# Performance work log

Measured on AMD Instinct MI355X. Metric: run time of the kernel, lower is better.

The kernel has to match this reference:

```python
import jax, jax.numpy as jnp
import numpy as np
import math

D_MODEL = 1024
N_HEADS = 16
D_HEAD = D_MODEL // N_HEADS  # 64, even (required for RoPE)
MAX_LEN = 1024


def _rope_cache(max_len, d_head, dtype=jnp.float32):
    half = d_head // 2
    inv_freq = jnp.exp(jnp.arange(half, dtype=dtype) * (-math.log(10000.0) / half))
    angles = jnp.arange(max_len, dtype=dtype)[:, None] * inv_freq[None, :]  # [max_len, half]
    return jnp.cos(angles), jnp.sin(angles)


def _apply_rope(t, cos, sin):
    # t: [B, H, L, D]; rotate-by-halves variant (cat of halves, not interleave)
    L = t.shape[2]
    half = t.shape[-1] // 2
    c = cos[:L, :half][None, None, :, :].astype(t.dtype)
    s = sin[:L, :half][None, None, :, :].astype(t.dtype)
    t1, t2 = t[..., :half], t[..., half:]
    return jnp.concatenate([t1 * c - t2 * s, t1 * s + t2 * c], axis=-1)


def setup_inputs() -> dict:
    key = jax.random.key(0)
    ks = jax.random.split(key, 11)
    B, L = 4, 1024
    std = 1.0 / math.sqrt(D_MODEL)
    return {
        "queries": jax.random.normal(ks[0], (B, L, D_MODEL), jnp.float32),
        "keys": jax.random.normal(ks[1], (B, L, D_MODEL), jnp.float32),
        "values": jax.random.normal(ks[2], (B, L, D_MODEL), jnp.float32),
        "Wq": jax.random.normal(ks[3], (D_MODEL, D_MODEL), jnp.float32) * std,
        "bq": jnp.zeros((D_MODEL,), jnp.float32),
        "Wk": jax.random.normal(ks[4], (D_MODEL, D_MODEL), jnp.float32) * std,
        "bk": jnp.zeros((D_MODEL,), jnp.float32),
        "Wv": jax.random.normal(ks[5], (D_MODEL, D_MODEL), jnp.float32) * std,
        "bv": jnp.zeros((D_MODEL,), jnp.float32),
        "Wo": jax.random.normal(ks[6], (D_MODEL, D_MODEL), jnp.float32) * std,
        "bo": jnp.zeros((D_MODEL,), jnp.float32),
    }


def reference(queries, keys, values, Wq, bq, Wk, bk, Wv, bv, Wo, bo):
    B, L, _ = queries.shape
    S = keys.shape[1]
    H, Dh = N_HEADS, D_HEAD
    cos, sin = _rope_cache(MAX_LEN, Dh, queries.dtype)

    q = (queries @ Wq + bq).reshape(B, L, H, Dh).transpose(0, 2, 1, 3)  # [B,H,L,Dh]
    k = (keys @ Wk + bk).reshape(B, S, H, Dh).transpose(0, 2, 1, 3)
    v = (values @ Wv + bv).reshape(B, S, H, Dh).transpose(0, 2, 1, 3)

    q = _apply_rope(q, cos, sin)
    k = _apply_rope(k, cos, sin)

    scores = jnp.einsum('bhid,bhjd->bhij', q, k) / math.sqrt(Dh)
    attn = jax.nn.softmax(scores, axis=-1)  # dropout is identity in eval
    out = jnp.einsum('bhij,bhjd->bhid', attn, v)  # [B,H,L,Dh]
    out = out.transpose(0, 2, 1, 3).reshape(B, L, H * Dh)
    return out @ Wo + bo
```

## Files before the change

kernel.cpp:

```cpp
#include <hip/hip_runtime.h>
#include <math.h>

#define BB 4
#define LL 1024
#define HH 16
#define DH 64
#define DM 1024
#define MM (BB * LL)

typedef short bf16x8 __attribute__((ext_vector_type(8)));
typedef float f32x4  __attribute__((ext_vector_type(4)));
typedef unsigned short u16x4 __attribute__((ext_vector_type(4)));

__device__ __forceinline__ unsigned short f2bf(float x) {
    union { float f; unsigned u; } v; v.f = x;
    unsigned r = v.u + 0x7fff + ((v.u >> 16) & 1);
    return (unsigned short)(r >> 16);
}

__device__ __forceinline__ void gl2lds16(const unsigned short* g, unsigned short* l) {
    __builtin_amdgcn_global_load_lds(
        (const __attribute__((address_space(1))) unsigned int*)g,
        (__attribute__((address_space(3))) unsigned int*)l, 16, 0, 0);
}

__global__ __launch_bounds__(256) void cvt_bf16_kernel(
    const float* __restrict__ i0, const float* __restrict__ i1, const float* __restrict__ i2,
    unsigned short* __restrict__ o0, unsigned short* __restrict__ o1, unsigned short* __restrict__ o2)
{
    int z = blockIdx.z;
    const float* in = (z == 0) ? i0 : (z == 1) ? i1 : i2;
    unsigned short* out = (z == 0) ? o0 : (z == 1) ? o1 : o2;
    int i = (blockIdx.x * 256 + threadIdx.x) * 4;
    float4 f = *(const float4*)(in + i);
    u16x4 r;
    r.x = f2bf(f.x); r.y = f2bf(f.y); r.z = f2bf(f.z); r.w = f2bf(f.w);
    *(u16x4*)(out + i) = r;
}

__global__ __launch_bounds__(256) void transpose_w_kernel(
    const float* __restrict__ w0, const float* __restrict__ w1,
    const float* __restrict__ w2, const float* __restrict__ w3,
    unsigned short* __restrict__ t0, unsigned short* __restrict__ t1,
    unsigned short* __restrict__ t2, unsigned short* __restrict__ t3)
{
    int z = blockIdx.z;
    const float* in = (z == 0) ? w0 : (z == 1) ? w1 : (z == 2) ? w2 : w3;
    unsigned short* out = (z == 0) ? t0 : (z == 1) ? t1 : (z == 2) ? t2 : t3;
    __shared__ float tile[32][33];
    int tx = threadIdx.x & 31, ty = threadIdx.x >> 5;
    int c0 = blockIdx.x * 32, r0 = blockIdx.y * 32;
    #pragma unroll
    for (int j = 0; j < 32; j += 8)
        tile[ty + j][tx] = in[(size_t)(r0 + ty + j) * 1024 + c0 + tx];
    __syncthreads();
    #pragma unroll
    for (int j = 0; j < 32; j += 8)
        out[(size_t)(c0 + ty + j) * 1024 + r0 + tx] = f2bf(tile[tx][ty + j]);
}

__global__ __launch_bounds__(256) void transpose_v_kernel(
    const unsigned short* __restrict__ v, unsigned short* __restrict__ vt)
{
    __shared__ unsigned short T[64][72];
    int bh = blockIdx.y, l0 = blockIdx.x * 64;
    const unsigned short* vg = v + ((size_t)bh * LL + l0) * DH;
    #pragma unroll
    for (int ii = 0; ii < 2; ++ii) {
        int i = ii * 256 + threadIdx.x;
        int r = i >> 3, cb = i & 7;
        bf16x8 vv = *(const bf16x8*)(vg + (size_t)r * DH + cb * 8);
        #pragma unroll
        for (int j = 0; j < 8; ++j)
            T[cb * 8 + j][r] = (unsigned short)vv[j];
    }
    __syncthreads();
    unsigned short* og = vt + (size_t)bh * DH * LL + l0;
    #pragma unroll
    for (int ii = 0; ii < 2; ++ii) {
        int i = ii * 256 + threadIdx.x;
        int d = i >> 3, lb = i & 7;
        *(bf16x8*)(og + (size_t)d * LL + lb * 8) = *(const bf16x8*)&T[d][lb * 8];
    }
}

__device__ __forceinline__ void gemm128_core(
    const unsigned short* __restrict__ A, const unsigned short* __restrict__ Bt,
    unsigned short* As, unsigned short* Bs, int tM, int tN, f32x4 (&acc)[4][4])
{
    const int tid  = threadIdx.x;
    const int wave = tid >> 6, lane = tid & 63;
    const int g = lane >> 4, lm = lane & 15;
    const int wm = wave >> 1, wn = wave & 1;
    const int lr = lane >> 3, lk = lane & 7;
    const int kbl = lk ^ lr;

    for (int kt = 0; kt < 16; ++kt) {
        const int k0 = kt * 64;
        if (kt) __syncthreads();
        #pragma unroll
        for (int it = 0; it < 4; ++it) {
            int rbase = wave * 32 + it * 8;
            int r = rbase + lr;
            gl2lds16(A  + (size_t)(tM + r) * 1024 + k0 + kbl * 8, As + rbase * 64);
            gl2lds16(Bt + (size_t)(tN + r) * 1024 + k0 + kbl * 8, Bs + rbase * 64);
        }
        __syncthreads();

        #pragma unroll
        for (int kk = 0; kk < 2; ++kk) {
            bf16x8 a[4], b[4];
            const int sw = ((kk * 4 + g) ^ (lm & 7)) * 8;
            #pragma unroll
            for (int mt = 0; mt < 4; ++mt)
                a[mt] = *(const bf16x8*)&As[(wm * 64 + mt * 16 + lm) * 64 + sw];
            #pragma unroll
            for (int nt = 0; nt < 4; ++nt)
                b[nt] = *(const bf16x8*)&Bs[(wn * 64 + nt * 16 + lm) * 64 + sw];
            #pragma unroll
            for (int mt = 0; mt < 4; ++mt)
                #pragma unroll
                for (int nt = 0; nt < 4; ++nt)
                    acc[mt][nt] = __builtin_amdgcn_mfma_f32_16x16x32_bf16(
                        a[mt], b[nt], acc[mt][nt], 0, 0, 0);
        }
    }
}

__global__ __launch_bounds__(256) void gemm_qkv_kernel(
    const unsigned short* __restrict__ Aq, const unsigned short* __restrict__ Ak,
    const unsigned short* __restrict__ Av,
    const unsigned short* __restrict__ Wqt, const unsigned short* __restrict__ Wkt,
    const unsigned short* __restrict__ Wvt,
    const float* __restrict__ bq, const float* __restrict__ bk, const float* __restrict__ bv,
    unsigned short* __restrict__ oq, unsigned short* __restrict__ ok,
    unsigned short* __restrict__ ov)
{
    __shared__ __align__(16) unsigned short As[128 * 64];
    __shared__ __align__(16) unsigned short Bs[128 * 64];

    const int z = blockIdx.z;
    const unsigned short* A  = (z == 0) ? Aq  : (z == 1) ? Ak  : Av;
    const unsigned short* Bt = (z == 0) ? Wqt : (z == 1) ? Wkt : Wvt;
    const float* bias        = (z == 0) ? bq  : (z == 1) ? bk  : bv;
    unsigned short* out      = (z == 0) ? oq  : (z == 1) ? ok  : ov;

    const int tM = blockIdx.y * 128, tN = blockIdx.x * 128;
    f32x4 acc[4][4] = {};
    gemm128_core(A, Bt, As, Bs, tM, tN, acc);

    const int wave = threadIdx.x >> 6, lane = threadIdx.x & 63;
    const int g = lane >> 4, lm = lane & 15;
    const int wm = wave >> 1, wn = wave & 1;

    const int colbase = tN + wn * 64;
    const int h = colbase >> 6;
    float bvv[4];
    #pragma unroll
    for (int nt = 0; nt < 4; ++nt) bvv[nt] = bias[colbase + nt * 16 + lm];

    if (z == 2) {
        #pragma unroll
        for (int mt = 0; mt < 4; ++mt)
            #pragma unroll
            for (int r = 0; r < 4; ++r) {
                int row = tM + wm * 64 + mt * 16 + g * 4 + r;
                int b = row >> 10, l = row & 1023;
                unsigned short* orow = out + ((size_t)(b * HH + h) * LL + l) * DH;
                #pragma unroll
                for (int nt = 0; nt < 4; ++nt)
                    orow[nt * 16 + lm] = f2bf(acc[mt][nt][r] + bvv[nt]);
            }
    } else {
        const float coef = -0.28782313662425583f;
        const float if0 = expf((float)lm * coef);
        const float if1 = expf((float)(lm + 16) * coef);
        const float sc  = (z == 0) ? 0.125f * 1.4426950408889634f : 1.0f;
        #pragma unroll
        for (int mt = 0; mt < 4; ++mt)
            #pragma unroll
            for (int r = 0; r < 4; ++r) {
                int row = tM + wm * 64 + mt * 16 + g * 4 + r;
                int b = row >> 10, l = row & 1023;
                unsigned short* orow = out + ((size_t)(b * HH + h) * LL + l) * DH;
                #pragma unroll
                for (int nt = 0; nt < 2; ++nt) {
                    float t1 = acc[mt][nt][r]     + bvv[nt];
                    float t2 = acc[mt][nt + 2][r] + bvv[nt + 2];
                    float ang = (float)l * (nt ? if1 : if0);
                    float s, c;
                    sincosf(ang, &s, &c);
                    orow[nt * 16 + lm]      = f2bf((t1 * c - t2 * s) * sc);
                    orow[nt * 16 + lm + 32] = f2bf((t1 * s + t2 * c) * sc);
                }
            }
    }
}

__global__ __launch_bounds__(256) void gemm_out_kernel(
    const unsigned short* __restrict__ A, const unsigned short* __restrict__ Bt,
    const float* __restrict__ bias, float* __restrict__ C)
{
    __shared__ __align__(16) unsigned short As[128 * 64];
    __shared__ __align__(16) unsigned short Bs[128 * 64];

    const int tM = blockIdx.y * 128, tN = blockIdx.x * 128;
    f32x4 acc[4][4] = {};
    gemm128_core(A, Bt, As, Bs, tM, tN, acc);

    const int wave = threadIdx.x >> 6, lane = threadIdx.x & 63;
    const int g = lane >> 4, lm = lane & 15;
    const int wm = wave >> 1, wn = wave & 1;

    float bvv[4];
    #pragma unroll
    for (int nt = 0; nt < 4; ++nt) bvv[nt] = bias[tN + wn * 64 + nt * 16 + lm];
    #pragma unroll
    for (int mt = 0; mt < 4; ++mt)
        #pragma unroll
        for (int r = 0; r < 4; ++r) {
            int row = tM + wm * 64 + mt * 16 + g * 4 + r;
            float* crow = C + (size_t)row * DM + tN + wn * 64;
            #pragma unroll
            for (int nt = 0; nt < 4; ++nt)
                crow[nt * 16 + lm] = acc[mt][nt][r] + bvv[nt];
        }
}

#define PSTR 72

__global__ __launch_bounds__(256) void attn_mfma_kernel(
    const unsigned short* __restrict__ q, const unsigned short* __restrict__ k,
    const unsigned short* __restrict__ vt, unsigned short* __restrict__ ctx)
{
    __shared__ __align__(16) unsigned short Ks[64 * 64];
    __shared__ __align__(16) unsigned short Vs[64 * 64];
    __shared__ __align__(16) unsigned short Pb[4][16 * PSTR];

    const int tid  = threadIdx.x;
    const int wave = tid >> 6, lane = tid & 63;
    const int g = lane >> 4, lm = lane & 15;
    const int lr = lane >> 3, lk = lane & 7;
    const int kbl = lk ^ lr;
    const int bh = blockIdx.y;
    const int qbase = blockIdx.x * 64;

    const unsigned short* qg  = q  + (size_t)(bh * LL + qbase) * DH;
    const unsigned short* kg  = k  + (size_t)bh * LL * DH;
    const unsigned short* vtg = vt + (size_t)bh * DH * LL;

    bf16x8 aq[2];
    {
        const unsigned short* qrow = qg + (wave * 16 + lm) * DH;
        aq[0] = *(const bf16x8*)(qrow + g * 8);
        aq[1] = *(const bf16x8*)(qrow + 32 + g * 8);
    }

    f32x4 acc[4] = {};
    float lrow[4] = {0.f, 0.f, 0.f, 0.f};

    for (int kt = 0; kt < 16; ++kt) {
        if (kt) __syncthreads();
        #pragma unroll
        for (int it = 0; it < 2; ++it) {
            int rbase = wave * 16 + it * 8;
            int r = rbase + lr;
            gl2lds16(kg  + (size_t)(kt * 64 + r) * DH + kbl * 8, Ks + rbase * 64);
            gl2lds16(vtg + (size_t)r * LL + kt * 64 + kbl * 8,  Vs + rbase * 64);
        }
        __syncthreads();

        f32x4 s[4] = {};
        #pragma unroll
        for (int kk = 0; kk < 2; ++kk) {
            const int sw = ((kk * 4 + g) ^ (lm & 7)) * 8;
            #pragma unroll
            for (int t = 0; t < 4; ++t) {
                bf16x8 bk = *(const bf16x8*)&Ks[(t * 16 + lm) * 64 + sw];
                s[t] = __builtin_amdgcn_mfma_f32_16x16x32_bf16(aq[kk], bk, s[t], 0, 0, 0);
            }
        }

        #pragma unroll
        for (int r = 0; r < 4; ++r) {
            float rs = 0.f;
            #pragma unroll
            for (int t = 0; t < 4; ++t) {
                float p = exp2f(s[t][r]);
                rs += p;
                Pb[wave][(g * 4 + r) * PSTR + t * 16 + lm] = f2bf(p);
            }
            lrow[r] += rs;
        }

        #pragma unroll
        for (int kk = 0; kk < 2; ++kk) {
            bf16x8 ap = *(const bf16x8*)&Pb[wave][lm * PSTR + kk * 32 + g * 8];
            #pragma unroll
            for (int dt = 0; dt < 4; ++dt) {
                bf16x8 bv = *(const bf16x8*)&Vs[(dt * 16 + lm) * 64
                                                + ((kk * 4 + g) ^ (lm & 7)) * 8];
                acc[dt] = __builtin_amdgcn_mfma_f32_16x16x32_bf16(ap, bv, acc[dt], 0, 0, 0);
            }
        }
    }

    int b = bh >> 4, h = bh & 15;
    #pragma unroll
    for (int r = 0; r < 4; ++r) {
        float ts = lrow[r];
        ts += __shfl_xor(ts, 1, 64);
        ts += __shfl_xor(ts, 2, 64);
        ts += __shfl_xor(ts, 4, 64);
        ts += __shfl_xor(ts, 8, 64);
        float inv = 1.f / ts;
        int qrow = qbase + wave * 16 + g * 4 + r;
        unsigned short* orow = ctx + (size_t)(b * LL + qrow) * DM + h * DH;
        #pragma unroll
        for (int dt = 0; dt < 4; ++dt)
            orow[dt * 16 + lm] = f2bf(acc[dt][r] * inv);
    }
}

extern "C" void kernel_launch(void* const* d_in, const int* in_sizes, int n_in,
                              void* d_out, int out_size, void* d_ws, size_t ws_size,
                              hipStream_t stream) {
    const float* queries = (const float*)d_in[0];
    const float* keys    = (const float*)d_in[1];
    const float* values  = (const float*)d_in[2];
    const float* Wq = (const float*)d_in[3];
    const float* bq = (const float*)d_in[4];
    const float* Wk = (const float*)d_in[5];
    const float* bk = (const float*)d_in[6];
    const float* Wv = (const float*)d_in[7];
    const float* bv = (const float*)d_in[8];
    const float* Wo = (const float*)d_in[9];
    const float* bo = (const float*)d_in[10];
    float* out = (float*)d_out;

    unsigned short* qb   = (unsigned short*)d_ws;
    unsigned short* kb_  = qb  + (size_t)MM * DM;
    unsigned short* vb_  = kb_ + (size_t)MM * DM;
    unsigned short* Wqt  = vb_ + (size_t)MM * DM;
    unsigned short* Wkt  = Wqt + (size_t)DM * DM;
    unsigned short* Wvt  = Wkt + (size_t)DM * DM;
    unsigned short* Wot  = Wvt + (size_t)DM * DM;
    unsigned short* q_ws = Wot + (size_t)DM * DM;
    unsigned short* k_ws = q_ws + (size_t)MM * DM;
    unsigned short* v_ws = k_ws + (size_t)MM * DM;
    unsigned short* ctx  = v_ws + (size_t)MM * DM;
    unsigned short* vt   = qb;

    cvt_bf16_kernel<<<dim3(MM * DM / 1024, 1, 3), 256, 0, stream>>>(
        queries, keys, values, qb, kb_, vb_);
    transpose_w_kernel<<<dim3(32, 32, 4), 256, 0, stream>>>(
        Wq, Wk, Wv, Wo, Wqt, Wkt, Wvt, Wot);
    gemm_qkv_kernel<<<dim3(DM / 128, MM / 128, 3), 256, 0, stream>>>(
        qb, kb_, vb_, Wqt, Wkt, Wvt, bq, bk, bv, q_ws, k_ws, v_ws);
    transpose_v_kernel<<<dim3(LL / 64, BB * HH), 256, 0, stream>>>(v_ws, vt);
    attn_mfma_kernel<<<dim3(LL / 64, BB * HH), 256, 0, stream>>>(
        q_ws, k_ws, vt, ctx);
    gemm_out_kernel<<<dim3(DM / 128, MM / 128), 256, 0, stream>>>(
        ctx, Wot, bo, out);
}
```

Measured before the change: 222.9 us.

## Fuse V transpose into QKV epilogue, precompute RoPE table, transpose S tile

The QKV GEMM epilogue now writes V directly in transposed [bh, d, l] layout with vectorized 4-element stores, which removes the separate transpose_v kernel and its round trip through memory. RoPE cos/sin values are precomputed once into a table by an extra z-slice of the convert kernel, replacing per-element sincosf in the epilogue with table loads. The attention kernel swaps the MFMA operands so each lane holds a query column, giving vectorized P stores and a cheaper row-sum reduction. Its grid is flattened so consecutive blocks handle different heads. The RoPE table lives in the ctx buffer, which is safe only because the attention kernel overwrites ctx after the QKV GEMM has finished reading the table.

Measured after the change: 222.3 us. No clear change (-0.3%).

```diff
diff --git a/kernel.cpp b/kernel.cpp
--- a/kernel.cpp
+++ b/kernel.cpp
@@ -26,9 +26,23 @@
 
 __global__ __launch_bounds__(256) void cvt_bf16_kernel(
     const float* __restrict__ i0, const float* __restrict__ i1, const float* __restrict__ i2,
-    unsigned short* __restrict__ o0, unsigned short* __restrict__ o1, unsigned short* __restrict__ o2)
+    unsigned short* __restrict__ o0, unsigned short* __restrict__ o1, unsigned short* __restrict__ o2,
+    float* __restrict__ ct, float* __restrict__ st)
 {
     int z = blockIdx.z;
+    if (z == 3) {
+        int idx = blockIdx.x * 256 + threadIdx.x;
+        if (idx < LL * 32) {
+            int l = idx >> 5, d = idx & 31;
+            const float coef = -0.28782313662425583f;
+            float ang = (float)l * expf((float)d * coef);
+            float s, c;
+            sincosf(ang, &s, &c);
+            ct[idx] = c;
+            st[idx] = s;
+        }
+        return;
+    }
     const float* in = (z == 0) ? i0 : (z == 1) ? i1 : i2;
     unsigned short* out = (z == 0) ? o0 : (z == 1) ? o1 : o2;
     int i = (blockIdx.x * 256 + threadIdx.x) * 4;
@@ -59,31 +73,6 @@
         out[(size_t)(c0 + ty + j) * 1024 + r0 + tx] = f2bf(tile[tx][ty + j]);
 }
 
-__global__ __launch_bounds__(256) void transpose_v_kernel(
-    const unsigned short* __restrict__ v, unsigned short* __restrict__ vt)
-{
-    __shared__ unsigned short T[64][72];
-    int bh = blockIdx.y, l0 = blockIdx.x * 64;
-    const unsigned short* vg = v + ((size_t)bh * LL + l0) * DH;
-    #pragma unroll
-    for (int ii = 0; ii < 2; ++ii) {
-        int i = ii * 256 + threadIdx.x;
-        int r = i >> 3, cb = i & 7;
-        bf16x8 vv = *(const bf16x8*)(vg + (size_t)r * DH + cb * 8);
-        #pragma unroll
-        for (int j = 0; j < 8; ++j)
-            T[cb * 8 + j][r] = (unsigned short)vv[j];
-    }
-    __syncthreads();
-    unsigned short* og = vt + (size_t)bh * DH * LL + l0;
-    #pragma unroll
-    for (int ii = 0; ii < 2; ++ii) {
-        int i = ii * 256 + threadIdx.x;
-        int d = i >> 3, lb = i & 7;
-        *(bf16x8*)(og + (size_t)d * LL + lb * 8) = *(const bf16x8*)&T[d][lb * 8];
-    }
-}
-
 __device__ __forceinline__ void gemm128_core(
     const unsigned short* __restrict__ A, const unsigned short* __restrict__ Bt,
     unsigned short* As, unsigned short* Bs, int tM, int tN, f32x4 (&acc)[4][4])
@@ -133,8 +122,9 @@
     const unsigned short* __restrict__ Wqt, const unsigned short* __restrict__ Wkt,
     const unsigned short* __restrict__ Wvt,
     const float* __restrict__ bq, const float* __restrict__ bk, const float* __restrict__ bv,
+    const float* __restrict__ ct, const float* __restrict__ st,
     unsigned short* __restrict__ oq, unsigned short* __restrict__ ok,
-    unsigned short* __restrict__ ov)
+    unsigned short* __restrict__ vt)
 {
     __shared__ __align__(16) unsigned short As[128 * 64];
     __shared__ __align__(16) unsigned short Bs[128 * 64];
@@ -143,7 +133,6 @@
     const unsigned short* A  = (z == 0) ? Aq  : (z == 1) ? Ak  : Av;
     const unsigned short* Bt = (z == 0) ? Wqt : (z == 1) ? Wkt : Wvt;
     const float* bias        = (z == 0) ? bq  : (z == 1) ? bk  : bv;
-    unsigned short* out      = (z == 0) ? oq  : (z == 1) ? ok  : ov;
 
     const int tM = blockIdx.y * 128, tN = blockIdx.x * 128;
     f32x4 acc[4][4] = {};
@@ -161,35 +150,37 @@
 
     if (z == 2) {
         #pragma unroll
+        for (int mt = 0; mt < 4; ++mt) {
+            int row0 = tM + wm * 64 + mt * 16 + g * 4;
+            int b = row0 >> 10, l0 = row0 & 1023;
+            #pragma unroll
+            for (int nt = 0; nt < 4; ++nt) {
+                int dloc = nt * 16 + lm;
+                u16x4 p4;
+                #pragma unroll
+                for (int r = 0; r < 4; ++r)
+                    p4[r] = f2bf(acc[mt][nt][r] + bvv[nt]);
+                *(u16x4*)(vt + (((size_t)(b * HH + h) * DH + dloc) << 10) + l0) = p4;
+            }
+        }
+    } else {
+        unsigned short* out = (z == 0) ? oq : ok;
+        const float sc = (z == 0) ? 0.125f * 1.4426950408889634f : 1.0f;
+        #pragma unroll
         for (int mt = 0; mt < 4; ++mt)
             #pragma unroll
             for (int r = 0; r < 4; ++r) {
                 int row = tM + wm * 64 + mt * 16 + g * 4 + r;
                 int b = row >> 10, l = row & 1023;
-                unsigned short* orow = out + ((size_t)(b * HH + h) * LL + l) * DH;
-                #pragma unroll
-                for (int nt = 0; nt < 4; ++nt)
-                    orow[nt * 16 + lm] = f2bf(acc[mt][nt][r] + bvv[nt]);
-            }
-    } else {
-        const float coef = -0.28782313662425583f;
-        const float if0 = expf((float)lm * coef);
-        const float if1 = expf((float)(lm + 16) * coef);
-        const float sc  = (z == 0) ? 0.125f * 1.4426950408889634f : 1.0f;
-        #pragma unroll
-        for (int mt = 0; mt < 4; ++mt)
-            #pragma unroll
-            for (int r = 0; r < 4; ++r) {
-                int row = tM + wm * 64 + mt * 16 + g * 4 + r;
-                int b = row >> 10, l = row & 1023;
+                const float* cl = ct + l * 32;
+                const float* sl = st + l * 32;
                 unsigned short* orow = out + ((size_t)(b * HH + h) * LL + l) * DH;
                 #pragma unroll
                 for (int nt = 0; nt < 2; ++nt) {
                     float t1 = acc[mt][nt][r]     + bvv[nt];
                     float t2 = acc[mt][nt + 2][r] + bvv[nt + 2];
-                    float ang = (float)l * (nt ? if1 : if0);
-                    float s, c;
-                    sincosf(ang, &s, &c);
+                    float c = cl[nt * 16 + lm];
+                    float s = sl[nt * 16 + lm];
                     orow[nt * 16 + lm]      = f2bf((t1 * c - t2 * s) * sc);
                     orow[nt * 16 + lm + 32] = f2bf((t1 * s + t2 * c) * sc);
                 }
@@ -242,8 +233,9 @@
     const int g = lane >> 4, lm = lane & 15;
     const int lr = lane >> 3, lk = lane & 7;
     const int kbl = lk ^ lr;
-    const int bh = blockIdx.y;
-    const int qbase = blockIdx.x * 64;
+    const int n = blockIdx.x;
+    const int bh = n & 63;
+    const int qbase = (n >> 6) * 64;
 
     const unsigned short* qg  = q  + (size_t)(bh * LL + qbase) * DH;
     const unsigned short* kg  = k  + (size_t)bh * LL * DH;
@@ -257,7 +249,7 @@
     }
 
     f32x4 acc[4] = {};
-    float lrow[4] = {0.f, 0.f, 0.f, 0.f};
+    float lsum = 0.f;
 
     for (int kt = 0; kt < 16; ++kt) {
         if (kt) __syncthreads();
@@ -276,44 +268,43 @@
             const int sw = ((kk * 4 + g) ^ (lm & 7)) * 8;
             #pragma unroll
             for (int t = 0; t < 4; ++t) {
-                bf16x8 bk = *(const bf16x8*)&Ks[(t * 16 + lm) * 64 + sw];
-                s[t] = __builtin_amdgcn_mfma_f32_16x16x32_bf16(aq[kk], bk, s[t], 0, 0, 0);
-            }
-        }
-
-        #pragma unroll
-        for (int r = 0; r < 4; ++r) {
-            float rs = 0.f;
-            #pragma unroll
-            for (int t = 0; t < 4; ++t) {
+                bf16x8 ak = *(const bf16x8*)&Ks[(t * 16 + lm) * 64 + sw];
+                s[t] = __builtin_amdgcn_mfma_f32_16x16x32_bf16(ak, aq[kk], s[t], 0, 0, 0);
+            }
+        }
+
+        #pragma unroll
+        for (int t = 0; t < 4; ++t) {
+            u16x4 p4;
+            #pragma unroll
+            for (int r = 0; r < 4; ++r) {
                 float p = exp2f(s[t][r]);
-                rs += p;
-                Pb[wave][(g * 4 + r) * PSTR + t * 16 + lm] = f2bf(p);
-            }
-            lrow[r] += rs;
+                lsum += p;
+                p4[r] = f2bf(p);
+            }
+            *(u16x4*)&Pb[wave][lm * PSTR + t * 16 + g * 4] = p4;
         }
 
         #pragma unroll
         for (int kk = 0; kk < 2; ++kk) {
+            const int sw = ((kk * 4 + g) ^ (lm & 7)) * 8;
             bf16x8 ap = *(const bf16x8*)&Pb[wave][lm * PSTR + kk * 32 + g * 8];
             #pragma unroll
             for (int dt = 0; dt < 4; ++dt) {
-                bf16x8 bv = *(const bf16x8*)&Vs[(dt * 16 + lm) * 64
-                                                + ((kk * 4 + g) ^ (lm & 7)) * 8];
+                bf16x8 bv = *(const bf16x8*)&Vs[(dt * 16 + lm) * 64 + sw];
                 acc[dt] = __builtin_amdgcn_mfma_f32_16x16x32_bf16(ap, bv, acc[dt], 0, 0, 0);
             }
         }
     }
 
+    float ts = lsum;
+    ts += __shfl_xor(ts, 16, 64);
+    ts += __shfl_xor(ts, 32, 64);
+
     int b = bh >> 4, h = bh & 15;
     #pragma unroll
     for (int r = 0; r < 4; ++r) {
-        float ts = lrow[r];
-        ts += __shfl_xor(ts, 1, 64);
-        ts += __shfl_xor(ts, 2, 64);
-        ts += __shfl_xor(ts, 4, 64);
-        ts += __shfl_xor(ts, 8, 64);
-        float inv = 1.f / ts;
+        float inv = 1.f / __shfl(ts, g * 4 + r, 64);
         int qrow = qbase + wave * 16 + g * 4 + r;
         unsigned short* orow = ctx + (size_t)(b * LL + qrow) * DM + h * DH;
         #pragma unroll
@@ -347,18 +338,19 @@
     unsigned short* Wot  = Wvt + (size_t)DM * DM;
     unsigned short* q_ws = Wot + (size_t)DM * DM;
     unsigned short* k_ws = q_ws + (size_t)MM * DM;
-    unsigned short* v_ws = k_ws + (size_t)MM * DM;
-    unsigned short* ctx  = v_ws + (size_t)MM * DM;
-    unsigned short* vt   = qb;
-
-    cvt_bf16_kernel<<<dim3(MM * DM / 1024, 1, 3), 256, 0, stream>>>(
-        queries, keys, values, qb, kb_, vb_);
+    unsigned short* vt   = k_ws + (size_t)MM * DM;
+    unsigned short* ctx  = vt   + (size_t)MM * DM;
+    float* rope_cos = (float*)ctx;
+    float* rope_sin = rope_cos + LL * 32;
+
+    cvt_bf16_kernel<<<dim3(MM * DM / 1024, 1, 4), 256, 0, stream>>>(
+        queries, keys, values, qb, kb_, vb_, rope_cos, rope_sin);
     transpose_w_kernel<<<dim3(32, 32, 4), 256, 0, stream>>>(
         Wq, Wk, Wv, Wo, Wqt, Wkt, Wvt, Wot);
     gemm_qkv_kernel<<<dim3(DM / 128, MM / 128, 3), 256, 0, stream>>>(
-        qb, kb_, vb_, Wqt, Wkt, Wvt, bq, bk, bv, q_ws, k_ws, v_ws);
-    transpose_v_kernel<<<dim3(LL / 64, BB * HH), 256, 0, stream>>>(v_ws, vt);
-    attn_mfma_kernel<<<dim3(LL / 64, BB * HH), 256, 0, stream>>>(
+        qb, kb_, vb_, Wqt, Wkt, Wvt, bq, bk, bv, rope_cos, rope_sin,
+        q_ws, k_ws, vt);
+    attn_mfma_kernel<<<dim3(LL / 64 * BB * HH), 256, 0, stream>>>(
         q_ws, k_ws, vt, ctx);
     gemm_out_kernel<<<dim3(DM / 128, MM / 128), 256, 0, stream>>>(
         ctx, Wot, bo, out);
```
